# Optimization experiments

Measured on AMD Instinct MI355X. Metric: run time of the kernel, lower is better.

## Reference

```python
import jax, jax.numpy as jnp
import numpy as np
import math

B, S, HID = 4, 2048, 1024
NH = 16
HD = HID // NH  # 64
DH = math.sqrt(HD)


def setup_inputs() -> dict:
    key = jax.random.key(0)
    ks = jax.random.split(key, 7)
    scale = 1.0 / math.sqrt(HID)
    return {
        "hidden_states": jax.random.normal(ks[0], (B, S, HID), dtype=jnp.float32),
        "Wq": jax.random.normal(ks[1], (HID, HID), dtype=jnp.float32) * scale,
        "bq": jnp.zeros((HID,), dtype=jnp.float32),
        "Wk": jax.random.normal(ks[2], (HID, HID), dtype=jnp.float32) * scale,
        "bk": jnp.zeros((HID,), dtype=jnp.float32),
        "Wv": jax.random.normal(ks[3], (HID, HID), dtype=jnp.float32) * scale,
        "bv": jnp.zeros((HID,), dtype=jnp.float32),
        "attention_mask": jnp.ones((B, S), dtype=jnp.int32),
    }


def _heads(x):
    # [B,S,HID] -> [B,NH,S,HD]
    b, s, _ = x.shape
    return x.reshape(b, s, NH, HD).transpose(0, 2, 1, 3)


def reference(hidden_states, Wq, bq, Wk, bk, Wv, bv, attention_mask):
    q = _heads(hidden_states @ Wq.T + bq)
    k = _heads(hidden_states @ Wk.T + bk)
    v = _heads(hidden_states @ Wv.T + bv)

    left_k = k / DH
    right_k = jax.nn.soft_sign(jax.nn.soft_sign(k) / DH) + v
    # scores: [B,NH,S,S]
    scores = jnp.einsum("bhqd,bhkd->bhqk", q, left_k + right_k) / DH
    # torch masks along the QUERY dim: mask[:, None, :, None] == 0 -> -10000
    scores = jnp.where(attention_mask[:, None, :, None] == 0, -10000.0, scores)
    probs = jax.nn.softmax(scores, axis=-1)
    ctx = jnp.einsum("bhqk,bhkd->bhqd", probs, v)
    # [B,NH,S,HD] -> [B,S,HID]
    return ctx.transpose(0, 2, 1, 3).reshape(hidden_states.shape[0], -1, HID)
```

## Files before the change

### kernel.cpp

```cpp
#include <hip/hip_runtime.h>
#include <hip/hip_fp16.h>
#include <cstdint>

#define B_   4
#define S_   2048
#define HID_ 1024
#define NH_  16
#define HD_  64
#define M_   (B_ * S_)

using f16   = _Float16;
using f16x4 = __attribute__((ext_vector_type(4))) _Float16;
using f16x8 = __attribute__((ext_vector_type(8))) _Float16;
using f32x4 = __attribute__((ext_vector_type(4))) float;
using u32x4 = __attribute__((ext_vector_type(4))) unsigned int;

__device__ __forceinline__ void g2lds16(const void* g, void* l) {
  __builtin_amdgcn_global_load_lds(
      (__attribute__((address_space(1))) void*)(uintptr_t)g,
      (__attribute__((address_space(3))) void*)(uint32_t)(uintptr_t)l,
      16, 0, 0);
}

__device__ __forceinline__ unsigned int pk16(float a, float b) {
  unsigned int r;
  asm("v_cvt_pkrtz_f16_f32 %0, %1, %2" : "=v"(r) : "v"(a), "v"(b));
  return r;
}

#define PIDX(r) (((r) & 32) | (((r) & 12) << 1) | ((((r) >> 4) & 1) << 2) | ((r) & 3))

__global__ void cvt_f32_f16_k(const float* __restrict__ src, f16* __restrict__ dst, int n4) {
  int i = blockIdx.x * blockDim.x + threadIdx.x;
  if (i >= n4) return;
  float4 v = ((const float4*)src)[i];
  f16x4 h;
  h[0] = (f16)v.x; h[1] = (f16)v.y; h[2] = (f16)v.z; h[3] = (f16)v.w;
  ((f16x4*)dst)[i] = h;
}

__global__ __launch_bounds__(256) void proj_gemm_k(
    const f16* __restrict__ A, const f16* __restrict__ W,
    const float* __restrict__ bq, const float* __restrict__ bk, const float* __restrict__ bv,
    f16* __restrict__ Out) {
  __shared__ __align__(16) f16 As[128 * 64];
  __shared__ __align__(16) f16 Bs[128 * 64];
  const int tid = threadIdx.x;
  const int l   = tid & 63;
  const int w   = tid >> 6;
  const int lr  = l & 15;
  const int lk  = (l >> 4) * 8;
  const int col0 = blockIdx.x * 128;
  const int row0 = blockIdx.y * 128;
  const int wr = (w >> 1) * 64;
  const int wc = (w & 1) * 64;

  f32x4 acc[4][4] = {};

  for (int kt = 0; kt < 16; ++kt) {
    const int k0 = kt * 64;
#pragma unroll
    for (int i = 0; i < 4; ++i) {
      const int c   = tid + i * 256;
      const int row = c >> 3;
      const int cb  = (c ^ row) & 7;
      g2lds16(A + (size_t)(row0 + row) * 1024 + k0 + cb * 8,
              As + (w * 64 + i * 256) * 8);
      g2lds16(W + (size_t)(col0 + row) * 1024 + k0 + cb * 8,
              Bs + (w * 64 + i * 256) * 8);
    }
    asm volatile("s_waitcnt vmcnt(0)" ::: "memory");
    __syncthreads();

#pragma unroll
    for (int kk = 0; kk < 64; kk += 32) {
      const int x = (kk + lk) >> 3;
      f16x8 af[4], bf[4];
#pragma unroll
      for (int m = 0; m < 4; ++m) {
        const int row = wr + m * 16 + lr;
        af[m] = *(const f16x8*)(As + (row * 8 + ((x ^ row) & 7)) * 8);
      }
#pragma unroll
      for (int n = 0; n < 4; ++n) {
        const int row = wc + n * 16 + lr;
        bf[n] = *(const f16x8*)(Bs + (row * 8 + ((x ^ row) & 7)) * 8);
      }
#pragma unroll
      for (int m = 0; m < 4; ++m)
#pragma unroll
        for (int n = 0; n < 4; ++n)
          acc[m][n] = __builtin_amdgcn_mfma_f32_16x16x32_f16(af[m], bf[n], acc[m][n], 0, 0, 0);
    }
    __syncthreads();
  }

  const int proj = col0 >> 10;
  const float* bias = (proj == 0) ? bq : ((proj == 1) ? bk : bv);
  f16* outp = Out + (size_t)proj * ((size_t)M_ * HID_);
#pragma unroll
  for (int n = 0; n < 4; ++n) {
    const int col = col0 + wc + n * 16 + lr;
    const int cp  = col & 1023;
    const float bb = bias[cp];
#pragma unroll
    for (int m = 0; m < 4; ++m) {
      const int rbase = row0 + wr + m * 16 + (l >> 4) * 4;
#pragma unroll
      for (int r = 0; r < 4; ++r)
        outp[(size_t)(rbase + r) * 1024 + cp] = (f16)(acc[m][n][r] + bb);
    }
  }
}

__global__ __launch_bounds__(256) void prep_kv_k(
    const f16* __restrict__ Kp, const f16* __restrict__ Vp,
    f16* __restrict__ Keff, f16* __restrict__ Vt) {
  const int bh = blockIdx.x;
  const int st = blockIdx.y;
  const int b = bh >> 4, h = bh & 15;
  const int tid = threadIdx.x;
  const float Cs = 0.180336880111120426f;
#pragma unroll
  for (int i = 0; i < 2; ++i) {
    const int c  = tid + i * 256;
    const int sl = c >> 3, cb = c & 7;
    const int s  = st * 64 + sl;
    const size_t src = (size_t)(b * S_ + s) * 1024 + h * 64 + cb * 8;
    const f16x8 kv = *(const f16x8*)(Kp + src);
    const f16x8 vv = *(const f16x8*)(Vp + src);
    f16x8 ke;
#pragma unroll
    for (int j = 0; j < 8; ++j) {
      const float kf = (float)kv[j], vf = (float)vv[j];
      const float s1 = kf / (1.f + fabsf(kf));
      const float t  = s1 * 0.125f;
      const float s2 = t / (1.f + fabsf(t));
      ke[j] = (f16)((kf * 0.125f + s2 + vf) * Cs);
    }
    *(f16x8*)(Keff + ((size_t)bh * S_ + s) * 64 + cb * 8) = ke;
#pragma unroll
    for (int j = 0; j < 8; ++j)
      Vt[((size_t)bh * 64 + cb * 8 + j) * S_ + s] = vv[j];
  }
}

__global__ __launch_bounds__(128, 2) void attn_k(
    const f16* __restrict__ Q,
    const f16* __restrict__ Keff,
    const f16* __restrict__ Vt,
    const int* __restrict__ mask,
    float* __restrict__ Out) {
  __shared__ __align__(16) f16 Kl[2][64 * 64];
  __shared__ __align__(16) f16 Vl[2][64 * 64];
  const int bh = blockIdx.x, qt = blockIdx.y;
  const int b = bh >> 4, h = bh & 15;
  const int tid = threadIdx.x;
  const int l = tid & 63, w = tid >> 6;
  const int lr = l & 15, g = l >> 4;

  f16x8 qf[4][2];
#pragma unroll
  for (int qb = 0; qb < 4; ++qb) {
    const int qrow = qt * 128 + w * 64 + qb * 16 + lr;
    const f16* qs = Q + (size_t)(b * S_ + qrow) * 1024 + h * 64 + g * 8;
    qf[qb][0] = *(const f16x8*)(qs);
    qf[qb][1] = *(const f16x8*)(qs + 32);
    if (mask[b * S_ + qrow] == 0) {
      qf[qb][0] = (f16x8)(f16)0;
      qf[qb][1] = (f16x8)(f16)0;
    }
  }

  f32x4 ctx[4][4] = {};
  float lacc[4] = {0.f, 0.f, 0.f, 0.f};

#define STAGE(bf, kt2)                                                         \
  {                                                                            \
    _Pragma("unroll") for (int i = 0; i < 4; ++i) {                            \
      const int n = tid + i * 128;                                             \
      const int row = n >> 3, cl = n & 7;                                      \
      const int c = cl ^ (row & 7);                                            \
      g2lds16(Keff + ((size_t)bh * S_ + (kt2) * 64 + PIDX(row)) * 64 + c * 8,  \
              &Kl[bf][(w * 64 + i * 128) * 8]);                                \
      g2lds16(Vt + ((size_t)bh * 64 + row) * 2048 + (kt2) * 64 + c * 8,        \
              &Vl[bf][(w * 64 + i * 128) * 8]);                                \
    }                                                                          \
  }

  STAGE(0, 0);
  asm volatile("s_waitcnt vmcnt(0)" ::: "memory");
  __syncthreads();

  for (int kt = 0; kt < 32; ++kt) {
    const int cur = kt & 1;
    if (kt < 31) STAGE(cur ^ 1, kt + 1);

    f16x8 pf[4][2];
#pragma unroll
    for (int cbp = 0; cbp < 2; ++cbp) {
      f32x4 sv[4][2] = {};
      __builtin_amdgcn_s_setprio(1);
#pragma unroll
      for (int kk = 0; kk < 2; ++kk)
#pragma unroll
        for (int cc = 0; cc < 2; ++cc) {
          const int row = (cbp * 2 + cc) * 16 + lr;
          const f16x8 kf = *(const f16x8*)(&Kl[cur][(row * 8 + ((kk * 4 + g) ^ (row & 7))) * 8]);
#pragma unroll
          for (int qb = 0; qb < 4; ++qb)
            sv[qb][cc] = __builtin_amdgcn_mfma_f32_16x16x32_f16(kf, qf[qb][kk], sv[qb][cc], 0, 0, 0);
        }
      __builtin_amdgcn_s_setprio(0);
#pragma unroll
      for (int qb = 0; qb < 4; ++qb) {
        float pv[2][4];
        float s = 0.f;
#pragma unroll
        for (int cc = 0; cc < 2; ++cc)
#pragma unroll
          for (int r = 0; r < 4; ++r) {
            const float pe = exp2f(sv[qb][cc][r]);
            pv[cc][r] = pe;
            s += pe;
          }
        lacc[qb] += s;
        u32x4 pw = {pk16(pv[0][0], pv[0][1]), pk16(pv[0][2], pv[0][3]),
                    pk16(pv[1][0], pv[1][1]), pk16(pv[1][2], pv[1][3])};
        pf[qb][cbp] = __builtin_bit_cast(f16x8, pw);
      }
    }

    __builtin_amdgcn_s_setprio(1);
#pragma unroll
    for (int kk = 0; kk < 2; ++kk)
#pragma unroll
      for (int db = 0; db < 4; ++db) {
        const int row = db * 16 + lr;
        const f16x8 vf = *(const f16x8*)(&Vl[cur][(row * 8 + ((kk * 4 + g) ^ (row & 7))) * 8]);
#pragma unroll
        for (int qb = 0; qb < 4; ++qb)
          ctx[qb][db] = __builtin_amdgcn_mfma_f32_16x16x32_f16(vf, pf[qb][kk], ctx[qb][db], 0, 0, 0);
      }
    __builtin_amdgcn_s_setprio(0);

    asm volatile("s_waitcnt vmcnt(0)" ::: "memory");
    __syncthreads();
  }

#pragma unroll
  for (int qb = 0; qb < 4; ++qb) {
    float ls = lacc[qb];
    ls += __shfl_xor(ls, 16);
    ls += __shfl_xor(ls, 32);
    const float linv = 1.0f / ls;
    const int qrow = qt * 128 + w * 64 + qb * 16 + lr;
    float* op = Out + (size_t)(b * S_ + qrow) * 1024 + h * 64 + g * 4;
#pragma unroll
    for (int db = 0; db < 4; ++db) {
      f32x4 o = ctx[qb][db] * linv;
      *(f32x4*)(op + db * 16) = o;
    }
  }
}

extern "C" void kernel_launch(void* const* d_in, const int* in_sizes, int n_in,
                              void* d_out, int out_size, void* d_ws, size_t ws_size,
                              hipStream_t stream) {
  const float* hs = (const float*)d_in[0];
  const float* Wq = (const float*)d_in[1];
  const float* bq = (const float*)d_in[2];
  const float* Wk = (const float*)d_in[3];
  const float* bk = (const float*)d_in[4];
  const float* Wv = (const float*)d_in[5];
  const float* bv = (const float*)d_in[6];
  const int* mask = (const int*)d_in[7];
  float* out = (float*)d_out;

  f16* hsF  = (f16*)d_ws;
  f16* wF   = hsF + (size_t)M_ * HID_;
  f16* qF   = wF + 3ull * HID_ * HID_;
  f16* kF   = qF + (size_t)M_ * HID_;
  f16* vF   = kF + (size_t)M_ * HID_;
  f16* keff = vF + (size_t)M_ * HID_;
  f16* vt   = keff + (size_t)M_ * HID_;

  cvt_f32_f16_k<<<dim3((M_ * HID_) / 1024), 256, 0, stream>>>(hs, hsF, (M_ * HID_) / 4);
  cvt_f32_f16_k<<<dim3((HID_ * HID_) / 1024), 256, 0, stream>>>(Wq, wF, (HID_ * HID_) / 4);
  cvt_f32_f16_k<<<dim3((HID_ * HID_) / 1024), 256, 0, stream>>>(Wk, wF + (size_t)HID_ * HID_, (HID_ * HID_) / 4);
  cvt_f32_f16_k<<<dim3((HID_ * HID_) / 1024), 256, 0, stream>>>(Wv, wF + 2ull * (size_t)HID_ * HID_, (HID_ * HID_) / 4);

  proj_gemm_k<<<dim3(24, 64), 256, 0, stream>>>(hsF, wF, bq, bk, bv, qF);
  prep_kv_k<<<dim3(64, 32), 256, 0, stream>>>(kF, vF, keff, vt);
  attn_k<<<dim3(64, 16), 128, 0, stream>>>(qF, keff, vt, mask, out);
}
```

Measured before the change: 202.7 us.

## Halve attention query and key tiles to double grid size and occupancy

The attention kernel now processes 64 query rows per block (32 per wave) and 32-key tiles instead of 128 and 64. The grid doubles to 2048 blocks, LDS use is halved, and launch bounds request 4 blocks per SM, with swizzled staging reworked for the narrower V tiles. The intent is more waves in flight and better load balance across CUs. In exchange, K/V tiles are reloaded twice as often per query, and there are twice as many loop iterations, each with a barrier and less MFMA work to hide latency.

```diff
diff --git a/kernel.cpp b/kernel.cpp
--- a/kernel.cpp
+++ b/kernel.cpp
@@ -145,24 +145,24 @@
   }
 }
 
-__global__ __launch_bounds__(128, 2) void attn_k(
+__global__ __launch_bounds__(128, 4) void attn_k(
     const f16* __restrict__ Q,
     const f16* __restrict__ Keff,
     const f16* __restrict__ Vt,
     const int* __restrict__ mask,
     float* __restrict__ Out) {
-  __shared__ __align__(16) f16 Kl[2][64 * 64];
-  __shared__ __align__(16) f16 Vl[2][64 * 64];
+  __shared__ __align__(16) f16 Kl[2][32 * 64];
+  __shared__ __align__(16) f16 Vl[2][64 * 32];
   const int bh = blockIdx.x, qt = blockIdx.y;
   const int b = bh >> 4, h = bh & 15;
   const int tid = threadIdx.x;
   const int l = tid & 63, w = tid >> 6;
   const int lr = l & 15, g = l >> 4;
 
-  f16x8 qf[4][2];
-#pragma unroll
-  for (int qb = 0; qb < 4; ++qb) {
-    const int qrow = qt * 128 + w * 64 + qb * 16 + lr;
+  f16x8 qf[2][2];
+#pragma unroll
+  for (int qb = 0; qb < 2; ++qb) {
+    const int qrow = qt * 64 + w * 32 + qb * 16 + lr;
     const f16* qs = Q + (size_t)(b * S_ + qrow) * 1024 + h * 64 + g * 8;
     qf[qb][0] = *(const f16x8*)(qs);
     qf[qb][1] = *(const f16x8*)(qs + 32);
@@ -172,89 +172,86 @@
     }
   }
 
-  f32x4 ctx[4][4] = {};
-  float lacc[4] = {0.f, 0.f, 0.f, 0.f};
-
-#define STAGE(bf, kt2)                                                         \
-  {                                                                            \
-    _Pragma("unroll") for (int i = 0; i < 4; ++i) {                            \
-      const int n = tid + i * 128;                                             \
-      const int row = n >> 3, cl = n & 7;                                      \
-      const int c = cl ^ (row & 7);                                            \
-      g2lds16(Keff + ((size_t)bh * S_ + (kt2) * 64 + PIDX(row)) * 64 + c * 8,  \
-              &Kl[bf][(w * 64 + i * 128) * 8]);                                \
-      g2lds16(Vt + ((size_t)bh * 64 + row) * 2048 + (kt2) * 64 + c * 8,        \
-              &Vl[bf][(w * 64 + i * 128) * 8]);                                \
-    }                                                                          \
+  f32x4 ctx[2][4] = {};
+  float lacc[2] = {0.f, 0.f};
+
+#define STAGE(bf, kt2)                                                          \
+  {                                                                             \
+    _Pragma("unroll") for (int i = 0; i < 2; ++i) {                             \
+      const int kr = i * 16 + w * 8 + (l >> 3);                                 \
+      const int kc = (l & 7) ^ (kr & 7);                                        \
+      g2lds16(Keff + ((size_t)bh * S_ + (kt2) * 32 + PIDX(kr)) * 64 + kc * 8,   \
+              &Kl[bf][(i * 128 + w * 64) * 8]);                                 \
+      const int vr = i * 32 + w * 16 + (l >> 2);                                \
+      const int vc = (l & 3) ^ (vr & 3);                                        \
+      g2lds16(Vt + ((size_t)bh * 64 + vr) * 2048 + (kt2) * 32 + vc * 8,         \
+              &Vl[bf][(i * 128 + w * 64) * 8]);                                 \
+    }                                                                           \
   }
 
   STAGE(0, 0);
   asm volatile("s_waitcnt vmcnt(0)" ::: "memory");
   __syncthreads();
 
-  for (int kt = 0; kt < 32; ++kt) {
+  for (int kt = 0; kt < 64; ++kt) {
     const int cur = kt & 1;
-    if (kt < 31) STAGE(cur ^ 1, kt + 1);
-
-    f16x8 pf[4][2];
-#pragma unroll
-    for (int cbp = 0; cbp < 2; ++cbp) {
-      f32x4 sv[4][2] = {};
-      __builtin_amdgcn_s_setprio(1);
-#pragma unroll
-      for (int kk = 0; kk < 2; ++kk)
-#pragma unroll
-        for (int cc = 0; cc < 2; ++cc) {
-          const int row = (cbp * 2 + cc) * 16 + lr;
-          const f16x8 kf = *(const f16x8*)(&Kl[cur][(row * 8 + ((kk * 4 + g) ^ (row & 7))) * 8]);
-#pragma unroll
-          for (int qb = 0; qb < 4; ++qb)
-            sv[qb][cc] = __builtin_amdgcn_mfma_f32_16x16x32_f16(kf, qf[qb][kk], sv[qb][cc], 0, 0, 0);
-        }
-      __builtin_amdgcn_s_setprio(0);
-#pragma unroll
-      for (int qb = 0; qb < 4; ++qb) {
-        float pv[2][4];
-        float s = 0.f;
-#pragma unroll
-        for (int cc = 0; cc < 2; ++cc)
-#pragma unroll
-          for (int r = 0; r < 4; ++r) {
-            const float pe = exp2f(sv[qb][cc][r]);
-            pv[cc][r] = pe;
-            s += pe;
-          }
-        lacc[qb] += s;
-        u32x4 pw = {pk16(pv[0][0], pv[0][1]), pk16(pv[0][2], pv[0][3]),
-                    pk16(pv[1][0], pv[1][1]), pk16(pv[1][2], pv[1][3])};
-        pf[qb][cbp] = __builtin_bit_cast(f16x8, pw);
-      }
-    }
-
+    if (kt < 63) STAGE(cur ^ 1, kt + 1);
+
+    f32x4 sv[2][2] = {};
     __builtin_amdgcn_s_setprio(1);
 #pragma unroll
     for (int kk = 0; kk < 2; ++kk)
 #pragma unroll
-      for (int db = 0; db < 4; ++db) {
-        const int row = db * 16 + lr;
-        const f16x8 vf = *(const f16x8*)(&Vl[cur][(row * 8 + ((kk * 4 + g) ^ (row & 7))) * 8]);
-#pragma unroll
-        for (int qb = 0; qb < 4; ++qb)
-          ctx[qb][db] = __builtin_amdgcn_mfma_f32_16x16x32_f16(vf, pf[qb][kk], ctx[qb][db], 0, 0, 0);
+      for (int cc = 0; cc < 2; ++cc) {
+        const int row = cc * 16 + lr;
+        const f16x8 kf = *(const f16x8*)(&Kl[cur][(row * 8 + ((kk * 4 + g) ^ (row & 7))) * 8]);
+#pragma unroll
+        for (int qb = 0; qb < 2; ++qb)
+          sv[qb][cc] = __builtin_amdgcn_mfma_f32_16x16x32_f16(kf, qf[qb][kk], sv[qb][cc], 0, 0, 0);
       }
     __builtin_amdgcn_s_setprio(0);
 
+    f16x8 pf[2];
+#pragma unroll
+    for (int qb = 0; qb < 2; ++qb) {
+      float pv[2][4];
+      float s = 0.f;
+#pragma unroll
+      for (int cc = 0; cc < 2; ++cc)
+#pragma unroll
+        for (int r = 0; r < 4; ++r) {
+          const float pe = exp2f(sv[qb][cc][r]);
+          pv[cc][r] = pe;
+          s += pe;
+        }
+      lacc[qb] += s;
+      u32x4 pw = {pk16(pv[0][0], pv[0][1]), pk16(pv[0][2], pv[0][3]),
+                  pk16(pv[1][0], pv[1][1]), pk16(pv[1][2], pv[1][3])};
+      pf[qb] = __builtin_bit_cast(f16x8, pw);
+    }
+
+    __builtin_amdgcn_s_setprio(1);
+#pragma unroll
+    for (int db = 0; db < 4; ++db) {
+      const int row = db * 16 + lr;
+      const f16x8 vf = *(const f16x8*)(&Vl[cur][(row * 4 + (g ^ (row & 3))) * 8]);
+#pragma unroll
+      for (int qb = 0; qb < 2; ++qb)
+        ctx[qb][db] = __builtin_amdgcn_mfma_f32_16x16x32_f16(vf, pf[qb], ctx[qb][db], 0, 0, 0);
+    }
+    __builtin_amdgcn_s_setprio(0);
+
     asm volatile("s_waitcnt vmcnt(0)" ::: "memory");
     __syncthreads();
   }
 
 #pragma unroll
-  for (int qb = 0; qb < 4; ++qb) {
+  for (int qb = 0; qb < 2; ++qb) {
     float ls = lacc[qb];
     ls += __shfl_xor(ls, 16);
     ls += __shfl_xor(ls, 32);
     const float linv = 1.0f / ls;
-    const int qrow = qt * 128 + w * 64 + qb * 16 + lr;
+    const int qrow = qt * 64 + w * 32 + qb * 16 + lr;
     float* op = Out + (size_t)(b * S_ + qrow) * 1024 + h * 64 + g * 4;
 #pragma unroll
     for (int db = 0; db < 4; ++db) {
@@ -292,5 +289,5 @@
 
   proj_gemm_k<<<dim3(24, 64), 256, 0, stream>>>(hsF, wF, bq, bk, bv, qF);
   prep_kv_k<<<dim3(64, 32), 256, 0, stream>>>(kF, vF, keff, vt);
-  attn_k<<<dim3(64, 16), 128, 0, stream>>>(qF, keff, vt, mask, out);
-}
+  attn_k<<<dim3(64, 32), 128, 0, stream>>>(qF, keff, vt, mask, out);
+}
```

Measured after the change: 207.0 us. 2.1% more time.
